# Kernel optimization log

Hardware: AMD Instinct MI355X
Metric: run time of the kernel (lower is better)

Reference implementation:

```python
import jax, jax.numpy as jnp
import numpy as np
import math

B, S, H, D = 2, 2048, 12, 64
DIM = H * D
TOTAL = B * S


def setup_inputs() -> dict:
    key = jax.random.key(0)
    ks = jax.random.split(key, 5)
    hidden_states = jax.random.normal(ks[0], (TOTAL, DIM), dtype=jnp.float32)
    Wqkv_w = jax.random.normal(ks[1], (3 * DIM, DIM), dtype=jnp.float32) * (1.0 / math.sqrt(DIM))
    Wqkv_b = jax.random.normal(ks[2], (3 * DIM,), dtype=jnp.float32) * 0.02
    bias = jax.random.normal(ks[3], (B, H, S, S), dtype=jnp.float32) * 0.1
    slopes = jax.random.uniform(ks[4], (H,), dtype=jnp.float32)
    cu_seqlens = jnp.array([0, S, 2 * S], dtype=jnp.int32)
    indices = jnp.arange(TOTAL, dtype=jnp.int64)
    attn_mask = jnp.ones((B, S), dtype=jnp.int32)
    return {"hidden_states": hidden_states, "Wqkv_w": Wqkv_w, "Wqkv_b": Wqkv_b,
            "bias": bias, "slopes": slopes, "cu_seqlens": cu_seqlens,
            "indices": indices, "attn_mask": attn_mask, "max_seqlen": S}


def reference(hidden_states, Wqkv_w, Wqkv_b, bias, slopes, cu_seqlens, indices, attn_mask, max_seqlen):
    total_nnz, dim = hidden_states.shape
    batch = cu_seqlens.shape[0] - 1
    # fused QKV projection (torch Linear: x @ W.T + b)
    qkv = hidden_states @ Wqkv_w.T + Wqkv_b  # (total_nnz, 3*dim)
    # pad_input: scatter unpadded rows into (batch*max_seqlen, 3*dim)
    padded = jnp.zeros((batch * max_seqlen, 3 * dim), dtype=qkv.dtype).at[indices].set(qkv)
    qkv = padded.reshape(batch, max_seqlen, 3, H, D)
    q = qkv[:, :, 0].transpose(0, 2, 1, 3)  # (b, h, s, d)
    k = qkv[:, :, 1].transpose(0, 2, 1, 3)
    v = qkv[:, :, 2].transpose(0, 2, 1, 3)
    scores = jnp.einsum('bhqd,bhkd->bhqk', q, k) / math.sqrt(D)
    scores = scores + bias  # ALiBi (dense bias tensor)
    probs = jax.nn.softmax(scores, axis=-1)  # dropout p=0 -> identity
    attn = jnp.einsum('bhqk,bhkd->bhqd', probs, v)
    attn = attn.transpose(0, 2, 1, 3).reshape(batch * max_seqlen, dim)
    # unpad_input_only: gather valid rows back
    return attn[indices]
```

## Files before the change

kernel.cpp:

```cpp
#include <hip/hip_runtime.h>


typedef __attribute__((ext_vector_type(8))) short short8;
typedef __attribute__((ext_vector_type(4))) float floatx4;
typedef unsigned short u16;
typedef unsigned int u32;

#define LOG2E 1.4426950408889634f

__device__ __forceinline__ u16 f2bf(float f) {
  u32 u = __float_as_uint(f);
  u += 0x7FFFu + ((u >> 16) & 1u);
  return (u16)(u >> 16);
}

typedef const __attribute__((address_space(1))) u32* gp_t;
typedef __attribute__((address_space(3))) u32* lp_t;
__device__ __forceinline__ void async_cp16(const void* g, void* l) {
  __builtin_amdgcn_global_load_lds((gp_t)g, (lp_t)l, 16, 0, 0);
}

__global__ __launch_bounds__(256) void pack_kernel(
    const float* __restrict__ A, const float* __restrict__ W,
    u16* __restrict__ Abf, u16* __restrict__ Wbf) {
  unsigned u = blockIdx.x * 256u + threadIdx.x;
  const unsigned nA = 786432u;
  float4 v;
  u16* dst;
  if (u < nA) { v = ((const float4*)A)[u]; dst = Abf + u * 4; }
  else        { unsigned q = u - nA; v = ((const float4*)W)[q]; dst = Wbf + q * 4; }
  ushort4 o;
  o.x = f2bf(v.x); o.y = f2bf(v.y); o.z = f2bf(v.z); o.w = f2bf(v.w);
  *(ushort4*)dst = o;
}

__global__ __launch_bounds__(256, 3) void qkv_gemm(
    const u16* __restrict__ Abf, const u16* __restrict__ Wbf,
    const float* __restrict__ bq,
    u16* __restrict__ Qb, u16* __restrict__ Kb, u16* __restrict__ Vb) {
  __shared__ __align__(16) char smem[32768];
  char* As0 = smem;
  char* Bs0 = smem + 8192;
  char* As1 = smem + 16384;
  char* Bs1 = smem + 24576;
  const unsigned t = threadIdx.x;
  unsigned orig = blockIdx.y * 18u + blockIdx.x;
  unsigned wg = (orig & 7u) * 72u + (orig >> 3);
  const unsigned nblk = wg % 18u, mblk = wg / 18u;
  const unsigned w = t >> 6, l = t & 63, quad = l >> 4, c = l & 15;
  const unsigned wm = (w >> 1) * 64, wn = (w & 1) * 64;

  floatx4 acc[4][4] = {};

  const unsigned b0 = t, b1 = t + 256u;
  const unsigned r0 = b0 >> 2, ch0 = (b0 & 3u) ^ (r0 & 3u);
  const unsigned r1 = b1 >> 2, ch1 = (b1 & 3u) ^ (r1 & 3u);
  const char* gA0 = (const char*)Abf + (size_t)((mblk * 128 + r0) * 768) * 2 + ch0 * 16;
  const char* gA1 = (const char*)Abf + (size_t)((mblk * 128 + r1) * 768) * 2 + ch1 * 16;
  const char* gB0 = (const char*)Wbf + (size_t)((nblk * 128 + r0) * 768) * 2 + ch0 * 16;
  const char* gB1 = (const char*)Wbf + (size_t)((nblk * 128 + r1) * 768) * 2 + ch1 * 16;

  async_cp16(gA0, As0 + b0 * 16);
  async_cp16(gA1, As0 + b1 * 16);
  async_cp16(gB0, Bs0 + b0 * 16);
  async_cp16(gB1, Bs0 + b1 * 16);
  __syncthreads();

  for (unsigned kt = 0; kt < 24; ++kt) {
    char* Ac = (kt & 1u) ? As1 : As0;
    char* Bc = (kt & 1u) ? Bs1 : Bs0;
    if (kt + 1 < 24) {
      char* An = (kt & 1u) ? As0 : As1;
      char* Bn = (kt & 1u) ? Bs0 : Bs1;
      async_cp16(gA0 + (kt + 1) * 64, An + b0 * 16);
      async_cp16(gA1 + (kt + 1) * 64, An + b1 * 16);
      async_cp16(gB0 + (kt + 1) * 64, Bn + b0 * 16);
      async_cp16(gB1 + (kt + 1) * 64, Bn + b1 * 16);
    }
    short8 af[4], bf[4];
#pragma unroll
    for (int mt = 0; mt < 4; ++mt) {
      unsigned row = wm + mt * 16 + c;
      af[mt] = *(const short8*)(Ac + row * 64 + 16 * (quad ^ (row & 3u)));
    }
#pragma unroll
    for (int nt = 0; nt < 4; ++nt) {
      unsigned row = wn + nt * 16 + c;
      bf[nt] = *(const short8*)(Bc + row * 64 + 16 * (quad ^ (row & 3u)));
    }
#pragma unroll
    for (int mt = 0; mt < 4; ++mt)
#pragma unroll
      for (int nt = 0; nt < 4; ++nt)
        acc[mt][nt] = __builtin_amdgcn_mfma_f32_16x16x32_bf16(af[mt], bf[nt], acc[mt][nt], 0, 0, 0);
    __syncthreads();
  }

  float bqv[4];
#pragma unroll
  for (int nt = 0; nt < 4; ++nt) bqv[nt] = bq[nblk * 128 + wn + nt * 16 + c];
#pragma unroll
  for (int mt = 0; mt < 4; ++mt) {
#pragma unroll
    for (int r = 0; r < 4; ++r) {
      unsigned m = mblk * 128 + wm + mt * 16 + quad * 4 + r;
      unsigned bb = m >> 11, s = m & 2047u;
#pragma unroll
      for (int nt = 0; nt < 4; ++nt) {
        float val = acc[mt][nt][r] + bqv[nt];
        unsigned n = nblk * 128 + wn + nt * 16 + c;
        u16 bv = f2bf(val);
        if (n < 768u) {
          unsigned h = n >> 6, d = n & 63u;
          Qb[(((bb * 12 + h) * 2048 + s) << 6) + d] = bv;
        } else if (n < 1536u) {
          unsigned n2 = n - 768u, h = n2 >> 6, d = n2 & 63u;
          Kb[(((bb * 12 + h) * 2048 + s) << 6) + d] = bv;
        } else {
          unsigned n2 = n - 1536u, h = n2 >> 6, d = n2 & 63u;
          Vb[(((bb * 12 + h) << 6) + d) * 2048 + s] = bv;
        }
      }
    }
  }
}

__global__ __launch_bounds__(256, 3) void attn_kernel(
    const u16* __restrict__ Qb, const u16* __restrict__ Kb,
    const u16* __restrict__ Vb, const float* __restrict__ bias,
    float* __restrict__ out) {
  __shared__ __align__(16) char smem[49152];
  char* Qs  = smem;
  char* Ks0 = smem + 8192;
  char* Ks1 = smem + 16384;
  char* Vs0 = smem + 24576;
  char* Vs1 = smem + 32768;
  char* Ps  = smem + 40960;
  const unsigned t = threadIdx.x;
  unsigned wgid = (blockIdx.x & 7u) * 96u + (blockIdx.x >> 3);
  const unsigned bh = wgid >> 5, qt = wgid & 31u;
  const unsigned q0 = qt * 64;
  const unsigned w = t >> 6, l = t & 63, quad = l >> 4, c = l & 15;

  const unsigned b0 = t, b1 = t + 256u;
  const unsigned r0 = b0 >> 3, ch0 = (b0 & 7u) ^ (r0 & 7u);
  const unsigned r1 = b1 >> 3, ch1 = (b1 & 7u) ^ (r1 & 7u);

  const char* gK0 = (const char*)Kb + (size_t)(bh * 2048 + r0) * 128 + ch0 * 16;
  const char* gK1 = (const char*)Kb + (size_t)(bh * 2048 + r1) * 128 + ch1 * 16;
  const char* gV0 = (const char*)Vb + (size_t)(bh * 64 + r0) * 4096 + ch0 * 16;
  const char* gV1 = (const char*)Vb + (size_t)(bh * 64 + r1) * 4096 + ch1 * 16;
  const float* bias_base = bias + (size_t)(bh * 2048 + q0 + w * 16 + quad * 4) * 2048 + c;
  const unsigned pb = w * 2048u;

  async_cp16((const char*)Qb + (size_t)(bh * 2048 + q0 + r0) * 128 + ch0 * 16, Qs + b0 * 16);
  async_cp16((const char*)Qb + (size_t)(bh * 2048 + q0 + r1) * 128 + ch1 * 16, Qs + b1 * 16);
  async_cp16(gK0, Ks0 + b0 * 16);
  async_cp16(gK1, Ks0 + b1 * 16);
  async_cp16(gV0, Vs0 + b0 * 16);
  async_cp16(gV1, Vs0 + b1 * 16);
  float bvA[4][4], bvB[4][4];
#pragma unroll
  for (int tt = 0; tt < 4; ++tt)
#pragma unroll
    for (int r = 0; r < 4; ++r)
      bvA[tt][r] = bias_base[(size_t)r * 2048 + tt * 16];
  __syncthreads();

  short8 aq[2];
  {
    unsigned row = w * 16 + c;
    aq[0] = *(const short8*)(Qs + row * 128 + 16 * ((quad + 0u) ^ (row & 7u)));
    aq[1] = *(const short8*)(Qs + row * 128 + 16 * ((quad + 4u) ^ (row & 7u)));
  }

  float mrun[4] = {-1e30f, -1e30f, -1e30f, -1e30f};
  float lrun[4] = {0.f, 0.f, 0.f, 0.f};
  floatx4 oacc[4] = {};

  for (unsigned tix = 0; tix < 32; ++tix) {
    const unsigned k0 = tix * 64u;
    const char* Kc = (tix & 1u) ? Ks1 : Ks0;
    const char* Vc = (tix & 1u) ? Vs1 : Vs0;

    if (tix + 1 < 32) {
      char* Kn = (tix & 1u) ? Ks0 : Ks1;
      char* Vn = (tix & 1u) ? Vs0 : Vs1;
      async_cp16(gK0 + (size_t)(k0 + 64) * 128, Kn + b0 * 16);
      async_cp16(gK1 + (size_t)(k0 + 64) * 128, Kn + b1 * 16);
      async_cp16(gV0 + (size_t)(k0 + 64) * 2, Vn + b0 * 16);
      async_cp16(gV1 + (size_t)(k0 + 64) * 2, Vn + b1 * 16);
#pragma unroll
      for (int tt = 0; tt < 4; ++tt)
#pragma unroll
        for (int r = 0; r < 4; ++r)
          bvB[tt][r] = bias_base[(size_t)r * 2048 + (k0 + 64) + tt * 16];
    }

    floatx4 s4[4] = {};
    __builtin_amdgcn_s_setprio(1);
#pragma unroll
    for (int ds = 0; ds < 2; ++ds)
#pragma unroll
      for (int tt = 0; tt < 4; ++tt) {
        unsigned row = tt * 16 + c;
        short8 kf = *(const short8*)(Kc + row * 128 + 16 * (((unsigned)quad + 4u * ds) ^ (c & 7u)));
        s4[tt] = __builtin_amdgcn_mfma_f32_16x16x32_bf16(aq[ds], kf, s4[tt], 0, 0, 0);
      }
    __builtin_amdgcn_s_setprio(0);

    float alpha[4];
    float pr[4][4];
#pragma unroll
    for (int r = 0; r < 4; ++r) {
      float x0 = fmaf(bvA[0][r], 8.0f, s4[0][r]) * (LOG2E / 8.0f);
      float x1 = fmaf(bvA[1][r], 8.0f, s4[1][r]) * (LOG2E / 8.0f);
      float x2 = fmaf(bvA[2][r], 8.0f, s4[2][r]) * (LOG2E / 8.0f);
      float x3 = fmaf(bvA[3][r], 8.0f, s4[3][r]) * (LOG2E / 8.0f);
      float mx = fmaxf(fmaxf(x0, x1), fmaxf(x2, x3));
      mx = fmaxf(mx, __shfl_xor(mx, 1));
      mx = fmaxf(mx, __shfl_xor(mx, 2));
      mx = fmaxf(mx, __shfl_xor(mx, 4));
      mx = fmaxf(mx, __shfl_xor(mx, 8));
      float mn = fmaxf(mrun[r], mx);
      float a = __builtin_amdgcn_exp2f(mrun[r] - mn);
      mrun[r] = mn;
      float p0 = __builtin_amdgcn_exp2f(x0 - mn);
      float p1 = __builtin_amdgcn_exp2f(x1 - mn);
      float p2 = __builtin_amdgcn_exp2f(x2 - mn);
      float p3 = __builtin_amdgcn_exp2f(x3 - mn);
      pr[0][r] = p0; pr[1][r] = p1; pr[2][r] = p2; pr[3][r] = p3;
      float rs = (p0 + p1) + (p2 + p3);
      rs += __shfl_xor(rs, 1);
      rs += __shfl_xor(rs, 2);
      rs += __shfl_xor(rs, 4);
      rs += __shfl_xor(rs, 8);
      lrun[r] = lrun[r] * a + rs;
      alpha[r] = a;
    }
#pragma unroll
    for (int dt = 0; dt < 4; ++dt) {
      oacc[dt][0] *= alpha[0]; oacc[dt][1] *= alpha[1];
      oacc[dt][2] *= alpha[2]; oacc[dt][3] *= alpha[3];
    }

#pragma unroll
    for (int tt = 0; tt < 4; ++tt)
#pragma unroll
      for (int r = 0; r < 4; ++r) {
        unsigned qq = quad * 4 + r;
        unsigned off = pb + qq * 128 + 16 * (((unsigned)(2 * tt) + (c >> 3)) ^ (qq & 7u)) + 2 * (c & 7u);
        *(u16*)(Ps + off) = f2bf(pr[tt][r]);
      }
    asm volatile("s_waitcnt lgkmcnt(0)" ::: "memory");

    __builtin_amdgcn_s_setprio(1);
#pragma unroll
    for (int js = 0; js < 2; ++js) {
      short8 pf = *(const short8*)(Ps + pb + (l & 15) * 128 +
                                   16 * (((unsigned)quad + 4u * js) ^ ((l & 15) & 7u)));
#pragma unroll
      for (int dt = 0; dt < 4; ++dt) {
        unsigned row = dt * 16 + c;
        short8 vf = *(const short8*)(Vc + row * 128 + 16 * (((unsigned)quad + 4u * js) ^ (c & 7u)));
        oacc[dt] = __builtin_amdgcn_mfma_f32_16x16x32_bf16(pf, vf, oacc[dt], 0, 0, 0);
      }
    }
    __builtin_amdgcn_s_setprio(0);

    __syncthreads();

    if (tix + 1 < 32) {
#pragma unroll
      for (int tt = 0; tt < 4; ++tt)
#pragma unroll
        for (int r = 0; r < 4; ++r)
          bvA[tt][r] = bvB[tt][r];
    }
  }

  unsigned b_ = bh / 12u, h = bh % 12u;
#pragma unroll
  for (int r = 0; r < 4; ++r) {
    float li = 1.0f / lrun[r];
    unsigned qg = q0 + w * 16 + quad * 4 + r;
    float* op = out + (size_t)(b_ * 2048 + qg) * 768 + h * 64 + c;
#pragma unroll
    for (int dt = 0; dt < 4; ++dt) op[dt * 16] = oacc[dt][r] * li;
  }
}

extern "C" void kernel_launch(void* const* d_in, const int* in_sizes, int n_in,
                              void* d_out, int out_size, void* d_ws, size_t ws_size,
                              hipStream_t stream) {
  const float* hidden = (const float*)d_in[0];
  const float* Wqkv_w = (const float*)d_in[1];
  const float* Wqkv_b = (const float*)d_in[2];
  const float* bias   = (const float*)d_in[3];
  float* out = (float*)d_out;

  char* ws = (char*)d_ws;
  u16* Abf = (u16*)(ws);
  u16* Wbf = (u16*)(ws + 6291456);
  u16* Qb  = (u16*)(ws + 9830400);
  u16* Kb  = (u16*)(ws + 16121856);
  u16* Vb  = (u16*)(ws + 22413312);

  pack_kernel<<<4800, 256, 0, stream>>>(hidden, Wqkv_w, Abf, Wbf);
  qkv_gemm<<<dim3(18, 32), 256, 0, stream>>>(Abf, Wbf, Wqkv_b, Qb, Kb, Vb);
  attn_kernel<<<768, 256, 0, stream>>>(Qb, Kb, Vb, bias, out);
}
```

Baseline: 599.2 us.

## Split attention over key dimension into four partitions with a combine kernel

Measured after the change: 645.6 us. 7.8% more time.

```diff
diff --git a/kernel.cpp b/kernel.cpp
--- a/kernel.cpp
+++ b/kernel.cpp
@@ -125,84 +125,75 @@
   }
 }
 
-__global__ __launch_bounds__(256, 3) void attn_kernel(
+__global__ __launch_bounds__(256, 6) void attn_kernel(
     const u16* __restrict__ Qb, const u16* __restrict__ Kb,
     const u16* __restrict__ Vb, const float* __restrict__ bias,
-    float* __restrict__ out) {
-  __shared__ __align__(16) char smem[49152];
-  char* Qs  = smem;
-  char* Ks0 = smem + 8192;
-  char* Ks1 = smem + 16384;
-  char* Vs0 = smem + 24576;
-  char* Vs1 = smem + 32768;
-  char* Ps  = smem + 40960;
+    float* __restrict__ Op, float* __restrict__ Mp, float* __restrict__ Lp) {
+  __shared__ __align__(16) char smem[20480];
+  char* Ks0 = smem;
+  char* Ks1 = smem + 4096;
+  char* Vs0 = smem + 8192;
+  char* Vs1 = smem + 12288;
+  char* Ps  = smem + 16384;
   const unsigned t = threadIdx.x;
-  unsigned wgid = (blockIdx.x & 7u) * 96u + (blockIdx.x >> 3);
-  const unsigned bh = wgid >> 5, qt = wgid & 31u;
+  unsigned wgid = (blockIdx.x & 7u) * 384u + (blockIdx.x >> 3);
+  const unsigned bh = wgid >> 7;
+  const unsigned rem = wgid & 127u;
+  const unsigned qt = rem >> 2, sp = rem & 3u;
   const unsigned q0 = qt * 64;
   const unsigned w = t >> 6, l = t & 63, quad = l >> 4, c = l & 15;
 
-  const unsigned b0 = t, b1 = t + 256u;
-  const unsigned r0 = b0 >> 3, ch0 = (b0 & 7u) ^ (r0 & 7u);
-  const unsigned r1 = b1 >> 3, ch1 = (b1 & 7u) ^ (r1 & 7u);
-
-  const char* gK0 = (const char*)Kb + (size_t)(bh * 2048 + r0) * 128 + ch0 * 16;
-  const char* gK1 = (const char*)Kb + (size_t)(bh * 2048 + r1) * 128 + ch1 * 16;
-  const char* gV0 = (const char*)Vb + (size_t)(bh * 64 + r0) * 4096 + ch0 * 16;
-  const char* gV1 = (const char*)Vb + (size_t)(bh * 64 + r1) * 4096 + ch1 * 16;
-  const float* bias_base = bias + (size_t)(bh * 2048 + q0 + w * 16 + quad * 4) * 2048 + c;
-  const unsigned pb = w * 2048u;
-
-  async_cp16((const char*)Qb + (size_t)(bh * 2048 + q0 + r0) * 128 + ch0 * 16, Qs + b0 * 16);
-  async_cp16((const char*)Qb + (size_t)(bh * 2048 + q0 + r1) * 128 + ch1 * 16, Qs + b1 * 16);
-  async_cp16(gK0, Ks0 + b0 * 16);
-  async_cp16(gK1, Ks0 + b1 * 16);
-  async_cp16(gV0, Vs0 + b0 * 16);
-  async_cp16(gV1, Vs0 + b1 * 16);
-  float bvA[4][4], bvB[4][4];
-#pragma unroll
-  for (int tt = 0; tt < 4; ++tt)
+  const unsigned rK = t >> 3, chK = (t & 7u) ^ (rK & 7u);
+  const unsigned rV = t >> 2, chV = (t & 3u) ^ (rV & 3u);
+
+  const char* gK = (const char*)Kb + (size_t)(bh * 2048 + sp * 512 + rK) * 128 + chK * 16;
+  const char* gV = (const char*)Vb + (size_t)(bh * 64 + rV) * 4096 + sp * 1024 + chV * 16;
+  const float* bias_base = bias + (size_t)(bh * 2048 + q0 + w * 16 + quad * 4) * 2048
+                                + sp * 512 + c;
+  const unsigned pb = w * 1024u;
+
+  async_cp16(gK, Ks0 + t * 16);
+  async_cp16(gV, Vs0 + t * 16);
+  short8 aq[2];
+  {
+    const u16* qrow = Qb + (size_t)(bh * 2048 + q0 + w * 16 + c) * 64 + quad * 8;
+    aq[0] = *(const short8*)(qrow);
+    aq[1] = *(const short8*)(qrow + 32);
+  }
+  float bvA[2][4], bvB[2][4];
+#pragma unroll
+  for (int tt = 0; tt < 2; ++tt)
 #pragma unroll
     for (int r = 0; r < 4; ++r)
       bvA[tt][r] = bias_base[(size_t)r * 2048 + tt * 16];
   __syncthreads();
 
-  short8 aq[2];
-  {
-    unsigned row = w * 16 + c;
-    aq[0] = *(const short8*)(Qs + row * 128 + 16 * ((quad + 0u) ^ (row & 7u)));
-    aq[1] = *(const short8*)(Qs + row * 128 + 16 * ((quad + 4u) ^ (row & 7u)));
-  }
-
   float mrun[4] = {-1e30f, -1e30f, -1e30f, -1e30f};
   float lrun[4] = {0.f, 0.f, 0.f, 0.f};
   floatx4 oacc[4] = {};
 
-  for (unsigned tix = 0; tix < 32; ++tix) {
-    const unsigned k0 = tix * 64u;
-    const char* Kc = (tix & 1u) ? Ks1 : Ks0;
-    const char* Vc = (tix & 1u) ? Vs1 : Vs0;
-
-    if (tix + 1 < 32) {
-      char* Kn = (tix & 1u) ? Ks0 : Ks1;
-      char* Vn = (tix & 1u) ? Vs0 : Vs1;
-      async_cp16(gK0 + (size_t)(k0 + 64) * 128, Kn + b0 * 16);
-      async_cp16(gK1 + (size_t)(k0 + 64) * 128, Kn + b1 * 16);
-      async_cp16(gV0 + (size_t)(k0 + 64) * 2, Vn + b0 * 16);
-      async_cp16(gV1 + (size_t)(k0 + 64) * 2, Vn + b1 * 16);
-#pragma unroll
-      for (int tt = 0; tt < 4; ++tt)
+  for (unsigned i = 0; i < 16; ++i) {
+    const char* Kc = (i & 1u) ? Ks1 : Ks0;
+    const char* Vc = (i & 1u) ? Vs1 : Vs0;
+
+    if (i + 1 < 16) {
+      char* Kn = (i & 1u) ? Ks0 : Ks1;
+      char* Vn = (i & 1u) ? Vs0 : Vs1;
+      async_cp16(gK + (size_t)(i + 1) * 4096, Kn + t * 16);
+      async_cp16(gV + (size_t)(i + 1) * 64, Vn + t * 16);
+#pragma unroll
+      for (int tt = 0; tt < 2; ++tt)
 #pragma unroll
         for (int r = 0; r < 4; ++r)
-          bvB[tt][r] = bias_base[(size_t)r * 2048 + (k0 + 64) + tt * 16];
-    }
-
-    floatx4 s4[4] = {};
+          bvB[tt][r] = bias_base[(size_t)r * 2048 + (i + 1) * 32 + tt * 16];
+    }
+
+    floatx4 s4[2] = {};
     __builtin_amdgcn_s_setprio(1);
 #pragma unroll
     for (int ds = 0; ds < 2; ++ds)
 #pragma unroll
-      for (int tt = 0; tt < 4; ++tt) {
+      for (int tt = 0; tt < 2; ++tt) {
         unsigned row = tt * 16 + c;
         short8 kf = *(const short8*)(Kc + row * 128 + 16 * (((unsigned)quad + 4u * ds) ^ (c & 7u)));
         s4[tt] = __builtin_amdgcn_mfma_f32_16x16x32_bf16(aq[ds], kf, s4[tt], 0, 0, 0);
@@ -210,14 +201,12 @@
     __builtin_amdgcn_s_setprio(0);
 
     float alpha[4];
-    float pr[4][4];
+    float pr[2][4];
 #pragma unroll
     for (int r = 0; r < 4; ++r) {
       float x0 = fmaf(bvA[0][r], 8.0f, s4[0][r]) * (LOG2E / 8.0f);
       float x1 = fmaf(bvA[1][r], 8.0f, s4[1][r]) * (LOG2E / 8.0f);
-      float x2 = fmaf(bvA[2][r], 8.0f, s4[2][r]) * (LOG2E / 8.0f);
-      float x3 = fmaf(bvA[3][r], 8.0f, s4[3][r]) * (LOG2E / 8.0f);
-      float mx = fmaxf(fmaxf(x0, x1), fmaxf(x2, x3));
+      float mx = fmaxf(x0, x1);
       mx = fmaxf(mx, __shfl_xor(mx, 1));
       mx = fmaxf(mx, __shfl_xor(mx, 2));
       mx = fmaxf(mx, __shfl_xor(mx, 4));
@@ -227,10 +216,8 @@
       mrun[r] = mn;
       float p0 = __builtin_amdgcn_exp2f(x0 - mn);
       float p1 = __builtin_amdgcn_exp2f(x1 - mn);
-      float p2 = __builtin_amdgcn_exp2f(x2 - mn);
-      float p3 = __builtin_amdgcn_exp2f(x3 - mn);
-      pr[0][r] = p0; pr[1][r] = p1; pr[2][r] = p2; pr[3][r] = p3;
-      float rs = (p0 + p1) + (p2 + p3);
+      pr[0][r] = p0; pr[1][r] = p1;
+      float rs = p0 + p1;
       rs += __shfl_xor(rs, 1);
       rs += __shfl_xor(rs, 2);
       rs += __shfl_xor(rs, 4);
@@ -245,24 +232,22 @@
     }
 
 #pragma unroll
-    for (int tt = 0; tt < 4; ++tt)
+    for (int tt = 0; tt < 2; ++tt)
 #pragma unroll
       for (int r = 0; r < 4; ++r) {
         unsigned qq = quad * 4 + r;
-        unsigned off = pb + qq * 128 + 16 * (((unsigned)(2 * tt) + (c >> 3)) ^ (qq & 7u)) + 2 * (c & 7u);
+        unsigned off = pb + qq * 64 + 16 * (((unsigned)(2 * tt) + (c >> 3)) ^ (qq & 3u)) + 2 * (c & 7u);
         *(u16*)(Ps + off) = f2bf(pr[tt][r]);
       }
     asm volatile("s_waitcnt lgkmcnt(0)" ::: "memory");
 
     __builtin_amdgcn_s_setprio(1);
-#pragma unroll
-    for (int js = 0; js < 2; ++js) {
-      short8 pf = *(const short8*)(Ps + pb + (l & 15) * 128 +
-                                   16 * (((unsigned)quad + 4u * js) ^ ((l & 15) & 7u)));
+    {
+      short8 pf = *(const short8*)(Ps + pb + (l & 15) * 64 + 16 * ((unsigned)quad ^ ((l & 15) & 3u)));
 #pragma unroll
       for (int dt = 0; dt < 4; ++dt) {
         unsigned row = dt * 16 + c;
-        short8 vf = *(const short8*)(Vc + row * 128 + 16 * (((unsigned)quad + 4u * js) ^ (c & 7u)));
+        short8 vf = *(const short8*)(Vc + row * 64 + 16 * ((unsigned)quad ^ (c & 3u)));
         oacc[dt] = __builtin_amdgcn_mfma_f32_16x16x32_bf16(pf, vf, oacc[dt], 0, 0, 0);
       }
     }
@@ -270,24 +255,50 @@
 
     __syncthreads();
 
-    if (tix + 1 < 32) {
-#pragma unroll
-      for (int tt = 0; tt < 4; ++tt)
+    if (i + 1 < 16) {
+#pragma unroll
+      for (int tt = 0; tt < 2; ++tt)
 #pragma unroll
         for (int r = 0; r < 4; ++r)
           bvA[tt][r] = bvB[tt][r];
     }
   }
 
-  unsigned b_ = bh / 12u, h = bh % 12u;
+  const unsigned pidx = (bh * 32u + qt) * 4u + sp;
 #pragma unroll
   for (int r = 0; r < 4; ++r) {
-    float li = 1.0f / lrun[r];
-    unsigned qg = q0 + w * 16 + quad * 4 + r;
-    float* op = out + (size_t)(b_ * 2048 + qg) * 768 + h * 64 + c;
-#pragma unroll
-    for (int dt = 0; dt < 4; ++dt) op[dt * 16] = oacc[dt][r] * li;
-  }
+    unsigned row = w * 16 + quad * 4 + r;
+    float* op = Op + (size_t)pidx * 4096 + row * 64 + c;
+#pragma unroll
+    for (int dt = 0; dt < 4; ++dt) op[dt * 16] = oacc[dt][r];
+    if (c == 0) {
+      Mp[pidx * 64 + row] = mrun[r];
+      Lp[pidx * 64 + row] = lrun[r];
+    }
+  }
+}
+
+__global__ __launch_bounds__(256) void combine_kernel(
+    const float* __restrict__ Op, const float* __restrict__ Mp,
+    const float* __restrict__ Lp, float* __restrict__ out) {
+  unsigned gid = blockIdx.x * 256u + threadIdx.x;
+  unsigned d = gid & 63u;
+  unsigned row = gid >> 6;
+  unsigned bh = row >> 11, q = row & 2047u;
+  unsigned qt = q >> 6, qr = q & 63u;
+  unsigned pidx0 = (bh * 32u + qt) * 4u;
+  size_t ob = (size_t)pidx0 * 4096 + qr * 64u + d;
+  unsigned mb = pidx0 * 64u + qr;
+  float m0 = Mp[mb], m1 = Mp[mb + 64], m2 = Mp[mb + 128], m3 = Mp[mb + 192];
+  float ms = fmaxf(fmaxf(m0, m1), fmaxf(m2, m3));
+  float w0 = __builtin_amdgcn_exp2f(m0 - ms);
+  float w1 = __builtin_amdgcn_exp2f(m1 - ms);
+  float w2 = __builtin_amdgcn_exp2f(m2 - ms);
+  float w3 = __builtin_amdgcn_exp2f(m3 - ms);
+  float den = w0 * Lp[mb] + w1 * Lp[mb + 64] + w2 * Lp[mb + 128] + w3 * Lp[mb + 192];
+  float num = w0 * Op[ob] + w1 * Op[ob + 4096] + w2 * Op[ob + 8192] + w3 * Op[ob + 12288];
+  unsigned b_ = bh / 12u, h = bh - b_ * 12u;
+  out[(size_t)(b_ * 2048 + q) * 768 + h * 64 + d] = num / den;
 }
 
 extern "C" void kernel_launch(void* const* d_in, const int* in_sizes, int n_in,
@@ -305,8 +316,12 @@
   u16* Qb  = (u16*)(ws + 9830400);
   u16* Kb  = (u16*)(ws + 16121856);
   u16* Vb  = (u16*)(ws + 22413312);
+  float* Op = (float*)(ws + 28704768);
+  float* Mp = (float*)(ws + 79036416);
+  float* Lp = (float*)(ws + 79822848);
 
   pack_kernel<<<4800, 256, 0, stream>>>(hidden, Wqkv_w, Abf, Wbf);
   qkv_gemm<<<dim3(18, 32), 256, 0, stream>>>(Abf, Wbf, Wqkv_b, Qb, Kb, Vb);
-  attn_kernel<<<768, 256, 0, stream>>>(Qb, Kb, Vb, bias, out);
-}
+  attn_kernel<<<3072, 256, 0, stream>>>(Qb, Kb, Vb, bias, Op, Mp, Lp);
+  combine_kernel<<<12288, 256, 0, stream>>>(Op, Mp, Lp, out);
+}
```
